# Kernel tuning notes

Measured on AMD Instinct MI355X. Metric: run time of the kernel, lower is better.

The kernel has to match this reference:

```python
import jax, jax.numpy as jnp
import numpy as np

RING_SIZES = list(range(3, 27, 2))  # 3,5,...,25 -> 12 rings; (1+12)*96 = 1248
BN_EPS = 1e-5


def _box_sum(x, k):
    """Sum over k x k window (k odd), 'same' zero padding. x: [B,C,H,W].
    O(1) per pixel via summed-area table instead of dense depthwise conv."""
    p = k // 2
    H, W = x.shape[2], x.shape[3]
    xp = jnp.pad(x, ((0, 0), (0, 0), (p, p), (p, p)))
    S = jnp.cumsum(jnp.cumsum(xp, axis=2), axis=3)
    S = jnp.pad(S, ((0, 0), (0, 0), (1, 0), (1, 0)))  # leading zero row/col
    return (S[:, :, k:k + H, k:k + W] - S[:, :, :H, k:k + W]
            - S[:, :, k:k + H, :W] + S[:, :, :H, :W])


def _ring_sum(x, k):
    """Depthwise conv with a k x k ring of ones == box(k) - box(k-2)."""
    inner = x if k == 3 else _box_sum(x, k - 2)
    return _box_sum(x, k) - inner


def _bn_eval(x, gamma, beta, mean, var):
    scale = gamma / jnp.sqrt(var + BN_EPS)
    return x * scale[None, :, None, None] + (beta - mean * scale)[None, :, None, None]


def _conv1x1(x, w, b):
    # x: [B,C,H,W], w: [O,C] -> [B,O,H,W]
    return jnp.einsum('bchw,oc->bohw', x, w) + b[None, :, None, None]


def setup_inputs() -> dict:
    key = jax.random.key(0)
    ks = jax.random.split(key, 13)
    B, C, H, W = 4, 96, 128, 128
    return {
        'x': jax.random.normal(ks[0], (B, C, H, W), jnp.float32),
        'bn1_gamma': jax.random.uniform(ks[1], (1248,), jnp.float32, 0.5, 1.5),
        'bn1_beta': jax.random.normal(ks[2], (1248,), jnp.float32) * 0.1,
        'bn1_mean': jax.random.normal(ks[3], (1248,), jnp.float32),
        'bn1_var': jax.random.uniform(ks[4], (1248,), jnp.float32, 0.5, 1.5),
        'conv1_w': jax.random.normal(ks[5], (512, 1248), jnp.float32) * (1.0 / np.sqrt(1248)),
        'conv1_b': jax.random.normal(ks[6], (512,), jnp.float32) * 0.01,
        'bn2_gamma': jax.random.uniform(ks[7], (512,), jnp.float32, 0.5, 1.5),
        'bn2_beta': jax.random.normal(ks[8], (512,), jnp.float32) * 0.1,
        'bn2_mean': jax.random.normal(ks[9], (512,), jnp.float32),
        'bn2_var': jax.random.uniform(ks[10], (512,), jnp.float32, 0.5, 1.5),
        'conv2_w': jax.random.normal(ks[11], (96, 512), jnp.float32) * (1.0 / np.sqrt(512)),
        'conv2_b': jax.random.normal(ks[12], (96,), jnp.float32) * 0.01,
    }


def reference(x, bn1_gamma, bn1_beta, bn1_mean, bn1_var, conv1_w, conv1_b,
              bn2_gamma, bn2_beta, bn2_mean, bn2_var, conv2_w, conv2_b):
    convs = [x] + [_ring_sum(x, k) for k in RING_SIZES]
    h = jnp.concatenate(convs, axis=1)  # [B, 1248, H, W]
    h = _bn_eval(h, bn1_gamma, bn1_beta, bn1_mean, bn1_var)
    h = jax.nn.relu(_conv1x1(h, conv1_w, conv1_b))
    h = _bn_eval(h, bn2_gamma, bn2_beta, bn2_mean, bn2_var)
    return _conv1x1(h, conv2_w, conv2_b)
```

## Files before the change

kernel.cpp:

```cpp
#include <hip/hip_runtime.h>
#include <hip/hip_bf16.h>
#include <cstdint>

typedef __attribute__((ext_vector_type(8))) short bf16x8;
typedef __attribute__((ext_vector_type(4))) short bf16x4;
typedef __attribute__((ext_vector_type(4))) float f32x4;

#define BN_EPS 1e-5f

__device__ __forceinline__ void sat_plane(const float* __restrict__ xp,
                                          float* __restrict__ Sg, int t)
{
  __shared__ float tile[16384];
  __shared__ float csA[512];
  __shared__ float csB[512];

  for (int i4 = t; i4 < 4096; i4 += 512) {
    int r = i4 >> 5;
    int g = i4 & 31;
    float4 v = *(const float4*)(xp + (size_t)r * 128 + g * 4);
    *(float4*)(tile + r * 128 + ((g ^ (r & 31)) << 2)) = v;
  }
  __syncthreads();

  int r = t & 127, ch = t >> 7;
  {
    float carry = 0.f;
#pragma unroll
    for (int g8 = 0; g8 < 8; ++g8) {
      int g = ch * 8 + g8;
      float* p = tile + r * 128 + ((g ^ (r & 31)) << 2);
      float4 v = *(float4*)p;
      float s0 = carry + v.x, s1 = s0 + v.y, s2 = s1 + v.z, s3 = s2 + v.w;
      float4 o; o.x = s0; o.y = s1; o.z = s2; o.w = s3;
      *(float4*)p = o;
      carry = s3;
    }
    csA[r * 4 + ch] = carry;
  }
  __syncthreads();
  if (ch > 0) {
    float offs = csA[r * 4 + 0];
    if (ch > 1) offs += csA[r * 4 + 1];
    if (ch > 2) offs += csA[r * 4 + 2];
#pragma unroll
    for (int g8 = 0; g8 < 8; ++g8) {
      int g = ch * 8 + g8;
      float* p = tile + r * 128 + ((g ^ (r & 31)) << 2);
      float4 v = *(float4*)p;
      v.x += offs; v.y += offs; v.z += offs; v.w += offs;
      *(float4*)p = v;
    }
  }
  __syncthreads();

  int xcol = t & 127, rc = t >> 7;
  int gc = xcol >> 2, wc = xcol & 3;
  float regs[32];
  {
    float run = 0.f;
#pragma unroll
    for (int r8 = 0; r8 < 32; ++r8) {
      int rr = rc * 32 + r8;
      run += tile[rr * 128 + ((gc ^ (rr & 31)) << 2) + wc];
      regs[r8] = run;
    }
    csB[xcol * 4 + rc] = run;
  }
  if (t < 132) Sg[t] = 0.f;
  if (t < 128) Sg[(t + 1) * 132] = 0.f;
  if (t < 128) {
    float* rp = Sg + (size_t)(t + 1) * 132;
    rp[129] = 0.f; rp[130] = 0.f; rp[131] = 0.f;
  }
  __syncthreads();

  float offs = 0.f;
  if (rc > 0) offs += csB[xcol * 4 + 0];
  if (rc > 1) offs += csB[xcol * 4 + 1];
  if (rc > 2) offs += csB[xcol * 4 + 2];
#pragma unroll
  for (int r8 = 0; r8 < 32; ++r8) {
    int rr = rc * 32 + r8;
    Sg[(rr + 1) * 132 + xcol + 1] = regs[r8] + offs;
  }
}

__global__ __launch_bounds__(512) void prepsat_kernel(
    const float* __restrict__ W1, const float* __restrict__ cb1,
    const float* __restrict__ g1, const float* __restrict__ be1,
    const float* __restrict__ mu1, const float* __restrict__ va1,
    const float* __restrict__ W2, const float* __restrict__ cb2,
    const float* __restrict__ g2, const float* __restrict__ be2,
    const float* __restrict__ mu2, const float* __restrict__ va2,
    const float* __restrict__ x,
    __hip_bfloat16* __restrict__ V, float* __restrict__ b1e,
    __hip_bfloat16* __restrict__ W2e, float* __restrict__ b2e,
    float* __restrict__ SAT, int nplanes)
{
  int blk = blockIdx.x;
  int t = threadIdx.x;
  if (blk < 512) {
    __shared__ float red[8];
    int o = blk;
    const float* wrow = W1 + (size_t)o * 1248;
    float acc = 0.f;
    for (int i = t; i < 1248; i += 512) {
      float s = g1[i] * rsqrtf(va1[i] + BN_EPS);
      float w = wrow[i];
      acc += w * (be1[i] - mu1[i] * s);
      float g = w * s;
      float gn = 0.f;
      if (i < 1152) {
        float sn = g1[i + 96] * rsqrtf(va1[i + 96] + BN_EPS);
        gn = wrow[i + 96] * sn;
      }
      V[(size_t)o * 1248 + i] = __float2bfloat16(g - gn);
    }
    for (int d = 32; d > 0; d >>= 1) acc += __shfl_down(acc, d);
    int lane = t & 63, wvv = t >> 6;
    if (lane == 0) red[wvv] = acc;
    __syncthreads();
    if (t == 0) {
      float s = cb1[o];
#pragma unroll
      for (int i = 0; i < 8; ++i) s += red[i];
      b1e[o] = s;
    }
  } else if (blk < 608) {
    __shared__ float red2[8];
    int o = blk - 512;
    const float* wrow = W2 + (size_t)o * 512;
    float acc;
    {
      int j = t;
      float s = g2[j] * rsqrtf(va2[j] + BN_EPS);
      float wv = wrow[j];
      acc = wv * (be2[j] - mu2[j] * s);
      W2e[(size_t)o * 512 + j] = __float2bfloat16(wv * s);
    }
    for (int d = 32; d > 0; d >>= 1) acc += __shfl_down(acc, d);
    int lane = t & 63, wvv = t >> 6;
    if (lane == 0) red2[wvv] = acc;
    __syncthreads();
    if (t == 0) {
      float s = cb2[o];
#pragma unroll
      for (int i = 0; i < 8; ++i) s += red2[i];
      b2e[o] = s;
    }
  } else {
    int plane = blk - 608;
    if (plane < nplanes)
      sat_plane(x + (size_t)plane * 16384, SAT + (size_t)plane * 17028, t);
  }
}

__global__ __launch_bounds__(512) void satonly_kernel(
    const float* __restrict__ x, float* __restrict__ SAT)
{
  sat_plane(x + (size_t)blockIdx.x * 16384,
            SAT + (size_t)blockIdx.x * 17028, threadIdx.x);
}

__global__ __launch_bounds__(512, 2) void fused4_kernel(
    const float* __restrict__ SAT, const __hip_bfloat16* __restrict__ V,
    const float* __restrict__ b1e, const __hip_bfloat16* __restrict__ W2e,
    const float* __restrict__ b2e, float* __restrict__ out, int nb, int b0)
{
  extern __shared__ __align__(16) char smem[];
  float* ET0 = (float*)smem;
  float* ET1 = (float*)(smem + 52000);
  __hip_bfloat16* As0 = (__hip_bfloat16*)(smem + 104000);
  __hip_bfloat16* As1 = (__hip_bfloat16*)(smem + 130624);

  int blk = blockIdx.x;
  int per_xcd = (nb * 128) >> 3;
  int r = (blk & 7) * per_xcd + (blk >> 3);
  int bL = r >> 7, y = r & 127;

  int t = threadIdx.x;
  int lane = t & 63, wv = t >> 6;
  int wo = wv >> 1, wp = wv & 1;
  int lr = lane & 15, quad = lane >> 4;
  int bpx = t & 127;
  int bg24 = t >> 7;

  const float* Sb = SAT + (size_t)bL * 96 * 17028;

  f32x4 acc[8][4];
#pragma unroll
  for (int io = 0; io < 8; ++io)
#pragma unroll
    for (int ip = 0; ip < 4; ++ip) acc[io][ip] = (f32x4){0.f, 0.f, 0.f, 0.f};

  float2 a2[4], a1[4], c2[4], c1[4];

  auto eload = [&](int jr, int h) {
    int y1 = ((y - jr < 0) ? 0 : (y - jr)) * 132;
    int y2 = (((y + jr > 127) ? 127 : (y + jr)) + 1) * 132;
    int n = h ? 4 : 3, base = h ? 1536 : 0;
#pragma unroll
    for (int k = 0; k < 4; ++k) {
      if (k >= n) break;
      int idx = base + t + 512 * k;
      if (idx < 3120) {
        int clp = idx / 65;
        int xq = idx - clp * 65;
        const float* p0 = Sb + (size_t)(2 * clp) * 17028 + 2 * xq;
        a2[k] = *(const float2*)(p0 + y2);
        a1[k] = *(const float2*)(p0 + y1);
        c2[k] = *(const float2*)(p0 + 17028 + y2);
        c1[k] = *(const float2*)(p0 + 17028 + y1);
      }
    }
  };

  auto ewrite = [&](float* ET, int h) {
    int n = h ? 4 : 3, base = h ? 1536 : 0;
#pragma unroll
    for (int k = 0; k < 4; ++k) {
      if (k >= n) break;
      int idx = base + t + 512 * k;
      if (idx < 3120) {
        int clp = idx / 65;
        int xq = idx - clp * 65;
        int xl = xq * 2, cl = clp * 2;
        int cw = cl ^ (((xl >> 3) & 7) << 2);
        float2 d0, d1;
        d0.x = a2[k].x - a1[k].x; d0.y = c2[k].x - c1[k].x;
        d1.x = a2[k].y - a1[k].y; d1.y = c2[k].y - c1[k].y;
        *(float2*)(ET + xl * 100 + cw) = d0;
        *(float2*)(ET + (xl + 1) * 100 + cw) = d1;
      }
    }
  };

  auto build_h = [&](const float* ET, __hip_bfloat16* As, int jr, int half) {
    int x2 = ((bpx + jr > 127) ? 127 : (bpx + jr)) + 1;
    int x1 = (bpx - jr < 0) ? 0 : (bpx - jr);
    int s2 = ((x2 >> 3) & 7) << 2;
    int s1 = ((x1 >> 3) & 7) << 2;
    const float* r2 = ET + x2 * 100;
    const float* r1 = ET + x1 * 100;
#pragma unroll
    for (int k = 0; k < 3; ++k) {
      int c = bg24 * 24 + half * 12 + 4 * k;
      float4 e2 = *(const float4*)(r2 + (c ^ s2));
      float4 e1 = *(const float4*)(r1 + (c ^ s1));
      union { bf16x4 v; __hip_bfloat16 hh[4]; } pk;
      pk.hh[0] = __float2bfloat16(e2.x - e1.x);
      pk.hh[1] = __float2bfloat16(e2.y - e1.y);
      pk.hh[2] = __float2bfloat16(e2.z - e1.z);
      pk.hh[3] = __float2bfloat16(e2.w - e1.w);
      *(bf16x4*)(As + bpx * 104 + c) = pk.v;
    }
  };

  auto mfma_sub = [&](int j, int sub, const __hip_bfloat16* As) {
    bf16x8 av[8], bs[4];
#pragma unroll
    for (int io = 0; io < 8; ++io)
      av[io] = *(const bf16x8*)(V + (size_t)(wo * 128 + io * 16 + lr) * 1248
                                + j * 96 + sub * 32 + quad * 8);
#pragma unroll
    for (int ip = 0; ip < 4; ++ip)
      bs[ip] = *(const bf16x8*)(As + (wp * 64 + ip * 16 + lr) * 104 + sub * 32 + quad * 8);
    __builtin_amdgcn_s_setprio(1);
#pragma unroll
    for (int io = 0; io < 8; ++io)
#pragma unroll
      for (int ip = 0; ip < 4; ++ip)
        acc[io][ip] = __builtin_amdgcn_mfma_f32_16x16x32_bf16(av[io], bs[ip], acc[io][ip], 0, 0, 0);
    __builtin_amdgcn_s_setprio(0);
  };

  eload(0, 0); ewrite(ET0, 0); eload(0, 1); ewrite(ET0, 1);
  __syncthreads();
  eload(1, 0); ewrite(ET1, 0);
  build_h(ET0, As0, 0, 0);
  eload(1, 1); ewrite(ET1, 1);
  build_h(ET0, As0, 0, 1);
  __syncthreads();

  for (int j = 0; j < 13; ++j) {
    float* ETw = (j & 1) ? ET1 : ET0;
    const float* ETr = (j & 1) ? ET0 : ET1;
    const __hip_bfloat16* Asr = (j & 1) ? As1 : As0;
    __hip_bfloat16* Asw = (j & 1) ? As0 : As1;
    bool pf = (j < 11), bd = (j < 12);
    if (pf) eload(j + 2, 0);
    mfma_sub(j, 0, Asr);
    if (pf) { ewrite(ETw, 0); eload(j + 2, 1); }
    if (bd) build_h(ETr, Asw, j + 1, 0);
    mfma_sub(j, 1, Asr);
    if (pf) ewrite(ETw, 1);
    if (bd) build_h(ETr, Asw, j + 1, 1);
    mfma_sub(j, 2, Asr);
    __syncthreads();
  }

  __hip_bfloat16* Yst = (__hip_bfloat16*)smem;
#pragma unroll
  for (int io = 0; io < 8; ++io) {
    int o1b = wo * 128 + io * 16 + quad * 4;
    float4 bias = *(const float4*)(b1e + o1b);
#pragma unroll
    for (int ip = 0; ip < 4; ++ip) {
      int pxx = wp * 64 + ip * 16 + lr;
      f32x4 a = acc[io][ip];
      float z0 = a[0] + bias.x; z0 = z0 > 0.f ? z0 : 0.f;
      float z1 = a[1] + bias.y; z1 = z1 > 0.f ? z1 : 0.f;
      float z2 = a[2] + bias.z; z2 = z2 > 0.f ? z2 : 0.f;
      float z3 = a[3] + bias.w; z3 = z3 > 0.f ? z3 : 0.f;
      union { bf16x4 v; __hip_bfloat16 hh[4]; } pk;
      pk.hh[0] = __float2bfloat16(z0); pk.hh[1] = __float2bfloat16(z1);
      pk.hh[2] = __float2bfloat16(z2); pk.hh[3] = __float2bfloat16(z3);
      *(bf16x4*)(Yst + pxx * 520 + o1b) = pk.v;
    }
  }
  __syncthreads();

  int og = wv >> 2;
  int pg = wv & 3;
  f32x4 acc2[3][2];
#pragma unroll
  for (int im = 0; im < 3; ++im)
#pragma unroll
    for (int tl = 0; tl < 2; ++tl) acc2[im][tl] = (f32x4){0.f, 0.f, 0.f, 0.f};

  for (int k2 = 0; k2 < 512; k2 += 32) {
    bf16x8 bfr2[2];
#pragma unroll
    for (int tl = 0; tl < 2; ++tl)
      bfr2[tl] = *(const bf16x8*)(Yst + (pg * 32 + tl * 16 + lr) * 520 + k2 + quad * 8);
#pragma unroll
    for (int im = 0; im < 3; ++im) {
      bf16x8 afr2 = *(const bf16x8*)(W2e + (size_t)(og * 48 + im * 16 + lr) * 512
                                     + k2 + quad * 8);
#pragma unroll
      for (int tl = 0; tl < 2; ++tl)
        acc2[im][tl] = __builtin_amdgcn_mfma_f32_16x16x32_bf16(afr2, bfr2[tl], acc2[im][tl], 0, 0, 0);
    }
  }

  size_t obase = ((size_t)(b0 + bL) * 96) * 16384 + (size_t)y * 128;
#pragma unroll
  for (int im = 0; im < 3; ++im) {
#pragma unroll
    for (int tl = 0; tl < 2; ++tl) {
      int pxx = pg * 32 + tl * 16 + lr;
#pragma unroll
      for (int rr = 0; rr < 4; ++rr) {
        int o2 = og * 48 + im * 16 + quad * 4 + rr;
        out[obase + (size_t)o2 * 16384 + pxx] = acc2[im][tl][rr] + b2e[o2];
      }
    }
  }
}

extern "C" void kernel_launch(void* const* d_in, const int* in_sizes, int n_in,
                              void* d_out, int out_size, void* d_ws, size_t ws_size,
                              hipStream_t stream)
{
  const float* x   = (const float*)d_in[0];
  const float* g1  = (const float*)d_in[1];
  const float* be1 = (const float*)d_in[2];
  const float* mu1 = (const float*)d_in[3];
  const float* va1 = (const float*)d_in[4];
  const float* W1  = (const float*)d_in[5];
  const float* cb1 = (const float*)d_in[6];
  const float* g2  = (const float*)d_in[7];
  const float* be2 = (const float*)d_in[8];
  const float* mu2 = (const float*)d_in[9];
  const float* va2 = (const float*)d_in[10];
  const float* W2  = (const float*)d_in[11];
  const float* cb2 = (const float*)d_in[12];
  float* out = (float*)d_out;

  hipFuncSetAttribute((const void*)fused4_kernel,
                      hipFuncAttributeMaxDynamicSharedMemorySize, 157248);

  char* w = (char*)d_ws;
  __hip_bfloat16* V   = (__hip_bfloat16*)w; w += (size_t)512 * 1248 * 2;
  __hip_bfloat16* W2e = (__hip_bfloat16*)w; w += (size_t)96 * 512 * 2;
  float* b1e = (float*)w; w += 2048;
  float* b2e = (float*)w; w += 512;
  size_t fixed = (size_t)(w - (char*)d_ws);

  const size_t satB = (size_t)96 * 17028 * 4;
  int nb = (ws_size >= fixed + 4 * satB + 4096) ? 4 : 1;

  float* SAT = (float*)w;

  if (nb == 4) {
    prepsat_kernel<<<992, 512, 0, stream>>>(W1, cb1, g1, be1, mu1, va1,
                                            W2, cb2, g2, be2, mu2, va2,
                                            x, V, b1e, W2e, b2e, SAT, 384);
    fused4_kernel<<<512, 512, 157248, stream>>>(SAT, V, b1e, W2e, b2e, out, 4, 0);
  } else {
    prepsat_kernel<<<608, 512, 0, stream>>>(W1, cb1, g1, be1, mu1, va1,
                                            W2, cb2, g2, be2, mu2, va2,
                                            x, V, b1e, W2e, b2e, SAT, 0);
    for (int b0 = 0; b0 < 4; ++b0) {
      satonly_kernel<<<96, 512, 0, stream>>>(x + (size_t)b0 * 96 * 16384, SAT);
      fused4_kernel<<<128, 512, 157248, stream>>>(SAT, V, b1e, W2e, b2e, out, 1, b0);
    }
  }
}
```

Baseline: 347.7 us.

## Store SAT row differences channel-major and vectorize loads in fused kernel

Changes the intermediate row-difference buffer from a pixel-major swizzled layout (x*100+channel) to a channel-major layout (channel*132+x). The SAT rows can then be fetched with float4 loads and no per-element divide by 65. The column-difference build step now reads eight channels per pixel with scalar LDS reads and writes one bf16x8 vector into an A tile whose row stride is padded to 108. The build and prefetch steps are also reordered within the pipeline. The aim is to cut global-load instruction count and integer index arithmetic, at the cost of more scalar LDS reads and possible bank conflicts in the build step.

```diff
diff --git a/kernel.cpp b/kernel.cpp
--- a/kernel.cpp
+++ b/kernel.cpp
@@ -163,28 +163,28 @@
             SAT + (size_t)blockIdx.x * 17028, threadIdx.x);
 }
 
-__global__ __launch_bounds__(512, 2) void fused4_kernel(
+__global__ __launch_bounds__(512, 2) void fused6_kernel(
     const float* __restrict__ SAT, const __hip_bfloat16* __restrict__ V,
     const float* __restrict__ b1e, const __hip_bfloat16* __restrict__ W2e,
     const float* __restrict__ b2e, float* __restrict__ out, int nb, int b0)
 {
   extern __shared__ __align__(16) char smem[];
-  float* ET0 = (float*)smem;
-  float* ET1 = (float*)(smem + 52000);
-  __hip_bfloat16* As0 = (__hip_bfloat16*)(smem + 104000);
-  __hip_bfloat16* As1 = (__hip_bfloat16*)(smem + 130624);
+  float* E0 = (float*)smem;
+  float* E1 = (float*)(smem + 50688);
+  __hip_bfloat16* As0 = (__hip_bfloat16*)(smem + 101376);
+  __hip_bfloat16* As1 = (__hip_bfloat16*)(smem + 129024);
 
   int blk = blockIdx.x;
-  int per_xcd = (nb * 128) >> 3;
-  int r = (blk & 7) * per_xcd + (blk >> 3);
+  int rows_per_xcd = (nb * 128) >> 3;
+  int r = (blk & 7) * rows_per_xcd + (blk >> 3);
   int bL = r >> 7, y = r & 127;
 
   int t = threadIdx.x;
   int lane = t & 63, wv = t >> 6;
   int wo = wv >> 1, wp = wv & 1;
   int lr = lane & 15, quad = lane >> 4;
-  int bpx = t & 127;
-  int bg24 = t >> 7;
+  int px = t & 127;
+  int bg = t >> 7;
 
   const float* Sb = SAT + (size_t)bL * 96 * 17028;
 
@@ -194,66 +194,52 @@
 #pragma unroll
     for (int ip = 0; ip < 4; ++ip) acc[io][ip] = (f32x4){0.f, 0.f, 0.f, 0.f};
 
-  float2 a2[4], a1[4], c2[4], c1[4];
+  float4 ea[3], eb[3];
+  float ta = 0.f, tb = 0.f;
 
   auto eload = [&](int jr, int h) {
     int y1 = ((y - jr < 0) ? 0 : (y - jr)) * 132;
     int y2 = (((y + jr > 127) ? 127 : (y + jr)) + 1) * 132;
-    int n = h ? 4 : 3, base = h ? 1536 : 0;
-#pragma unroll
-    for (int k = 0; k < 4; ++k) {
-      if (k >= n) break;
-      int idx = base + t + 512 * k;
-      if (idx < 3120) {
-        int clp = idx / 65;
-        int xq = idx - clp * 65;
-        const float* p0 = Sb + (size_t)(2 * clp) * 17028 + 2 * xq;
-        a2[k] = *(const float2*)(p0 + y2);
-        a1[k] = *(const float2*)(p0 + y1);
-        c2[k] = *(const float2*)(p0 + 17028 + y2);
-        c1[k] = *(const float2*)(p0 + 17028 + y1);
-      }
+#pragma unroll
+    for (int k = 0; k < 3; ++k) {
+      int idx = t + 512 * (h * 3 + k);
+      int cl = idx >> 5, ck = idx & 31;
+      const float* bp = Sb + (size_t)cl * 17028 + ck * 4;
+      ea[k] = *(const float4*)(bp + y2);
+      eb[k] = *(const float4*)(bp + y1);
+    }
+    if (h == 1 && t < 96) {
+      const float* bp = Sb + (size_t)t * 17028 + 128;
+      ta = bp[y2];
+      tb = bp[y1];
     }
   };
 
-  auto ewrite = [&](float* ET, int h) {
-    int n = h ? 4 : 3, base = h ? 1536 : 0;
-#pragma unroll
-    for (int k = 0; k < 4; ++k) {
-      if (k >= n) break;
-      int idx = base + t + 512 * k;
-      if (idx < 3120) {
-        int clp = idx / 65;
-        int xq = idx - clp * 65;
-        int xl = xq * 2, cl = clp * 2;
-        int cw = cl ^ (((xl >> 3) & 7) << 2);
-        float2 d0, d1;
-        d0.x = a2[k].x - a1[k].x; d0.y = c2[k].x - c1[k].x;
-        d1.x = a2[k].y - a1[k].y; d1.y = c2[k].y - c1[k].y;
-        *(float2*)(ET + xl * 100 + cw) = d0;
-        *(float2*)(ET + (xl + 1) * 100 + cw) = d1;
-      }
-    }
+  auto ewrite = [&](float* E, int h) {
+#pragma unroll
+    for (int k = 0; k < 3; ++k) {
+      int idx = t + 512 * (h * 3 + k);
+      int cl = idx >> 5, ck = idx & 31;
+      float4 d;
+      d.x = ea[k].x - eb[k].x; d.y = ea[k].y - eb[k].y;
+      d.z = ea[k].z - eb[k].z; d.w = ea[k].w - eb[k].w;
+      *(float4*)(E + cl * 132 + ck * 4) = d;
+    }
+    if (h == 1 && t < 96) E[t * 132 + 128] = ta - tb;
   };
 
-  auto build_h = [&](const float* ET, __hip_bfloat16* As, int jr, int half) {
-    int x2 = ((bpx + jr > 127) ? 127 : (bpx + jr)) + 1;
-    int x1 = (bpx - jr < 0) ? 0 : (bpx - jr);
-    int s2 = ((x2 >> 3) & 7) << 2;
-    int s1 = ((x1 >> 3) & 7) << 2;
-    const float* r2 = ET + x2 * 100;
-    const float* r1 = ET + x1 * 100;
-#pragma unroll
-    for (int k = 0; k < 3; ++k) {
-      int c = bg24 * 24 + half * 12 + 4 * k;
-      float4 e2 = *(const float4*)(r2 + (c ^ s2));
-      float4 e1 = *(const float4*)(r1 + (c ^ s1));
-      union { bf16x4 v; __hip_bfloat16 hh[4]; } pk;
-      pk.hh[0] = __float2bfloat16(e2.x - e1.x);
-      pk.hh[1] = __float2bfloat16(e2.y - e1.y);
-      pk.hh[2] = __float2bfloat16(e2.z - e1.z);
-      pk.hh[3] = __float2bfloat16(e2.w - e1.w);
-      *(bf16x4*)(As + bpx * 104 + c) = pk.v;
+  auto build_k = [&](const float* E, __hip_bfloat16* As, int jr, int k0, int k1) {
+    int x1 = (px - jr < 0) ? 0 : (px - jr);
+    int x2 = ((px + jr > 127) ? 127 : (px + jr)) + 1;
+#pragma unroll
+    for (int k = k0; k < k1; ++k) {
+      int g = bg + 4 * k;
+      const float* Eb = E + g * 8 * 132;
+      union { bf16x8 v; __hip_bfloat16 h8[8]; } pk;
+#pragma unroll
+      for (int i = 0; i < 8; ++i)
+        pk.h8[i] = __float2bfloat16(Eb[i * 132 + x2] - Eb[i * 132 + x1]);
+      *(bf16x8*)(As + px * 108 + g * 8) = pk.v;
     }
   };
 
@@ -265,7 +251,7 @@
                                 + j * 96 + sub * 32 + quad * 8);
 #pragma unroll
     for (int ip = 0; ip < 4; ++ip)
-      bs[ip] = *(const bf16x8*)(As + (wp * 64 + ip * 16 + lr) * 104 + sub * 32 + quad * 8);
+      bs[ip] = *(const bf16x8*)(As + (wp * 64 + ip * 16 + lr) * 108 + sub * 32 + quad * 8);
     __builtin_amdgcn_s_setprio(1);
 #pragma unroll
     for (int io = 0; io < 8; ++io)
@@ -275,27 +261,28 @@
     __builtin_amdgcn_s_setprio(0);
   };
 
-  eload(0, 0); ewrite(ET0, 0); eload(0, 1); ewrite(ET0, 1);
-  __syncthreads();
-  eload(1, 0); ewrite(ET1, 0);
-  build_h(ET0, As0, 0, 0);
-  eload(1, 1); ewrite(ET1, 1);
-  build_h(ET0, As0, 0, 1);
+  eload(0, 0); ewrite(E0, 0); eload(0, 1); ewrite(E0, 1);
+  __syncthreads();
+  eload(1, 0); ewrite(E1, 0);
+  build_k(E0, As0, 0, 0, 2);
+  eload(1, 1); ewrite(E1, 1);
+  build_k(E0, As0, 0, 2, 3);
   __syncthreads();
 
   for (int j = 0; j < 13; ++j) {
-    float* ETw = (j & 1) ? ET1 : ET0;
-    const float* ETr = (j & 1) ? ET0 : ET1;
+    float* Ew = (j & 1) ? E1 : E0;
+    const float* Er = (j & 1) ? E0 : E1;
     const __hip_bfloat16* Asr = (j & 1) ? As1 : As0;
     __hip_bfloat16* Asw = (j & 1) ? As0 : As1;
     bool pf = (j < 11), bd = (j < 12);
     if (pf) eload(j + 2, 0);
     mfma_sub(j, 0, Asr);
-    if (pf) { ewrite(ETw, 0); eload(j + 2, 1); }
-    if (bd) build_h(ETr, Asw, j + 1, 0);
+    if (pf) ewrite(Ew, 0);
+    if (bd) build_k(Er, Asw, j + 1, 0, 2);
+    if (pf) eload(j + 2, 1);
     mfma_sub(j, 1, Asr);
-    if (pf) ewrite(ETw, 1);
-    if (bd) build_h(ETr, Asw, j + 1, 1);
+    if (pf) ewrite(Ew, 1);
+    if (bd) build_k(Er, Asw, j + 1, 2, 3);
     mfma_sub(j, 2, Asr);
     __syncthreads();
   }
@@ -378,8 +365,8 @@
   const float* cb2 = (const float*)d_in[12];
   float* out = (float*)d_out;
 
-  hipFuncSetAttribute((const void*)fused4_kernel,
-                      hipFuncAttributeMaxDynamicSharedMemorySize, 157248);
+  hipFuncSetAttribute((const void*)fused6_kernel,
+                      hipFuncAttributeMaxDynamicSharedMemorySize, 156672);
 
   char* w = (char*)d_ws;
   __hip_bfloat16* V   = (__hip_bfloat16*)w; w += (size_t)512 * 1248 * 2;
@@ -397,14 +384,14 @@
     prepsat_kernel<<<992, 512, 0, stream>>>(W1, cb1, g1, be1, mu1, va1,
                                             W2, cb2, g2, be2, mu2, va2,
                                             x, V, b1e, W2e, b2e, SAT, 384);
-    fused4_kernel<<<512, 512, 157248, stream>>>(SAT, V, b1e, W2e, b2e, out, 4, 0);
+    fused6_kernel<<<512, 512, 156672, stream>>>(SAT, V, b1e, W2e, b2e, out, 4, 0);
   } else {
     prepsat_kernel<<<608, 512, 0, stream>>>(W1, cb1, g1, be1, mu1, va1,
                                             W2, cb2, g2, be2, mu2, va2,
                                             x, V, b1e, W2e, b2e, SAT, 0);
     for (int b0 = 0; b0 < 4; ++b0) {
       satonly_kernel<<<96, 512, 0, stream>>>(x + (size_t)b0 * 96 * 16384, SAT);
-      fused4_kernel<<<128, 512, 157248, stream>>>(SAT, V, b1e, W2e, b2e, out, 1, b0);
-    }
-  }
-}
+      fused6_kernel<<<128, 512, 156672, stream>>>(SAT, V, b1e, W2e, b2e, out, 1, b0);
+    }
+  }
+}
```

After: 283.4 us. 18.5% less time.
